# Optimization experiments

Measured on AMD Instinct MI355X. Metric: run time of the kernel, lower is better.

The kernel has to match this reference:

```python
import jax, jax.numpy as jnp
import numpy as np

N = 1024            # number of proposals (128 proposals x 8 images)
D_APP = 2048        # appearance feature dim
D_K = 128           # key/query/value dim
D_G = 128           # geometric embedding dim


def setup_inputs() -> dict:
    key = jax.random.key(0)
    ks = jax.random.split(key, 10)
    s_app = 1.0 / np.sqrt(D_APP)
    s_geo = 1.0 / np.sqrt(D_G)
    return {
        "app_feature": jax.random.normal(ks[0], (N, D_APP), jnp.float32),
        "position_embedding": jax.random.normal(ks[1], (N, N, D_G), jnp.float32),
        "WQ_w": jax.random.normal(ks[2], (D_K, D_APP), jnp.float32) * s_app,
        "WQ_b": jax.random.normal(ks[3], (D_K,), jnp.float32) * 0.01,
        "WK_w": jax.random.normal(ks[4], (D_K, D_APP), jnp.float32) * s_app,
        "WK_b": jax.random.normal(ks[5], (D_K,), jnp.float32) * 0.01,
        "WV_w": jax.random.normal(ks[6], (D_K, D_APP), jnp.float32) * s_app,
        "WV_b": jax.random.normal(ks[7], (D_K,), jnp.float32) * 0.01,
        "WG_w": jax.random.normal(ks[8], (1, D_G), jnp.float32) * s_geo,
        "WG_b": jax.random.normal(ks[9], (1,), jnp.float32) * 0.01,
    }


def reference(app_feature, position_embedding,
              WQ_w, WQ_b, WK_w, WK_b, WV_w, WV_b, WG_w, WG_b):
    n = app_feature.shape[0]
    dim_k = WQ_w.shape[0]
    # projections: (N, D_K)
    w_q = app_feature @ WQ_w.T + WQ_b
    w_k = app_feature @ WK_w.T + WK_b
    w_v = app_feature @ WV_w.T + WV_b
    # appearance scores: (N, N)
    scaled_dot = (w_q @ w_k.T) / jnp.sqrt(jnp.asarray(dim_k, app_feature.dtype))
    # geometric bias: Linear(D_G -> 1) + ReLU, reshaped to (N, N)
    w_g = jax.nn.relu(jnp.einsum('mng,g->mn', position_embedding, WG_w[0]) + WG_b[0])
    # additive bias then row-softmax
    w_mn = jax.nn.softmax(scaled_dot + w_g, axis=1)
    return w_mn @ w_v  # (N, D_K)
```

## Files before the change

kernel.cpp:

```cpp
#include <hip/hip_runtime.h>
#include <math.h>

#define N_PROP 1024
#define DAPP   2048
#define DK     128

__global__ __launch_bounds__(256) void init_bias_kernel(
    const float* __restrict__ bQ, const float* __restrict__ bK,
    const float* __restrict__ bV,
    float* __restrict__ Q, float* __restrict__ K, float* __restrict__ V) {
  int i = blockIdx.x * 256 + threadIdx.x;
  if (i < N_PROP * DK) {
    int c = i & (DK - 1);
    Q[i] = bQ[c];
    K[i] = bK[c];
    V[i] = bV[c];
  }
}

#define BM 64
#define BN 64
#define KC 32
#define KSPLIT_CHUNK 512

__global__ __launch_bounds__(256) void proj_kernel(
    const float* __restrict__ X,
    const float* __restrict__ WQ, const float* __restrict__ WK,
    const float* __restrict__ WV,
    float* __restrict__ Q, float* __restrict__ K, float* __restrict__ V) {
  __shared__ __attribute__((aligned(16))) float As[KC][BM + 4];
  __shared__ __attribute__((aligned(16))) float Bs[KC][BN + 4];

  const int nt = blockIdx.x;
  const int mt = blockIdx.y;
  const int kz = blockIdx.z;
  const int row0 = mt * BM;
  const int proj = nt >> 1;
  const int col0 = (nt & 1) * 64;

  const float* __restrict__ W = (proj == 0) ? WQ : ((proj == 1) ? WK : WV);
  float* __restrict__ O = (proj == 0) ? Q : ((proj == 1) ? K : V);

  const int t  = threadIdx.x;
  const int tx = t & 15, ty = t >> 4;
  const int kk = t & 31, mm = t >> 5;

  float acc[4][4] = {};

  const int k0base = kz * KSPLIT_CHUNK;
  for (int k0 = k0base; k0 < k0base + KSPLIT_CHUNK; k0 += KC) {
    __syncthreads();
#pragma unroll
    for (int r = 0; r < 8; ++r) {
      As[kk][mm + r * 8] = X[(size_t)(row0 + mm + r * 8) * DAPP + k0 + kk];
      Bs[kk][mm + r * 8] = W[(size_t)(col0 + mm + r * 8) * DAPP + k0 + kk];
    }
    __syncthreads();
#pragma unroll
    for (int k = 0; k < KC; ++k) {
      float4 a = *(const float4*)&As[k][ty * 4];
      float4 b = *(const float4*)&Bs[k][tx * 4];
      acc[0][0] += a.x * b.x; acc[0][1] += a.x * b.y; acc[0][2] += a.x * b.z; acc[0][3] += a.x * b.w;
      acc[1][0] += a.y * b.x; acc[1][1] += a.y * b.y; acc[1][2] += a.y * b.z; acc[1][3] += a.y * b.w;
      acc[2][0] += a.z * b.x; acc[2][1] += a.z * b.y; acc[2][2] += a.z * b.z; acc[2][3] += a.z * b.w;
      acc[3][0] += a.w * b.x; acc[3][1] += a.w * b.y; acc[3][2] += a.w * b.z; acc[3][3] += a.w * b.w;
    }
  }

#pragma unroll
  for (int i = 0; i < 4; ++i)
#pragma unroll
    for (int j = 0; j < 4; ++j)
      atomicAdd(&O[(size_t)(row0 + ty * 4 + i) * DK + col0 + tx * 4 + j],
                acc[i][j]);
}

__global__ __launch_bounds__(256) void score_kernel(
    const float* __restrict__ Q, const float* __restrict__ Kmat,
    float* __restrict__ S) {
  __shared__ __attribute__((aligned(16))) float As[KC][BM + 4];
  __shared__ __attribute__((aligned(16))) float Bs[KC][BN + 4];

  const int col0 = blockIdx.x * BN;
  const int row0 = blockIdx.y * BM;
  const int t  = threadIdx.x;
  const int tx = t & 15, ty = t >> 4;
  const int kk = t & 31, mm = t >> 5;

  float acc[4][4] = {};

  for (int k0 = 0; k0 < DK; k0 += KC) {
    __syncthreads();
#pragma unroll
    for (int r = 0; r < 8; ++r) {
      As[kk][mm + r * 8] = Q[(size_t)(row0 + mm + r * 8) * DK + k0 + kk];
      Bs[kk][mm + r * 8] = Kmat[(size_t)(col0 + mm + r * 8) * DK + k0 + kk];
    }
    __syncthreads();
#pragma unroll
    for (int k = 0; k < KC; ++k) {
      float4 a = *(const float4*)&As[k][ty * 4];
      float4 b = *(const float4*)&Bs[k][tx * 4];
      acc[0][0] += a.x * b.x; acc[0][1] += a.x * b.y; acc[0][2] += a.x * b.z; acc[0][3] += a.x * b.w;
      acc[1][0] += a.y * b.x; acc[1][1] += a.y * b.y; acc[1][2] += a.y * b.z; acc[1][3] += a.y * b.w;
      acc[2][0] += a.z * b.x; acc[2][1] += a.z * b.y; acc[2][2] += a.z * b.z; acc[2][3] += a.z * b.w;
      acc[3][0] += a.w * b.x; acc[3][1] += a.w * b.y; acc[3][2] += a.w * b.z; acc[3][3] += a.w * b.w;
    }
  }

  const float scale = 0.08838834764831845f;
#pragma unroll
  for (int i = 0; i < 4; ++i)
#pragma unroll
    for (int j = 0; j < 4; ++j)
      S[(size_t)(row0 + ty * 4 + i) * N_PROP + col0 + tx * 4 + j] =
          acc[i][j] * scale;
}

__global__ __launch_bounds__(256) void fused_gsm_pv_kernel(
    const float* __restrict__ pos, const float* __restrict__ S,
    const float* __restrict__ V, const float* __restrict__ wg,
    const float* __restrict__ bg, float* __restrict__ out) {
  __shared__ __attribute__((aligned(16))) float p[N_PROP];
  __shared__ __attribute__((aligned(16))) float4 accs[256];
  __shared__ float wred[4];

  const int m = blockIdx.x;
  const int t = threadIdx.x;
  const int l  = t & 31;
  const int hw = t >> 5;

  const float4 w4 = *(const float4*)&wg[l * 4];
  const float bG = bg[0];

  {
    const float* __restrict__ pr =
        pos + (size_t)m * N_PROP * DK + (size_t)(hw * 4) * DK + (l << 2);
#pragma unroll 4
    for (int it = 0; it < 32; ++it, pr += 32 * DK) {
      const float4 p0 = *(const float4*)(pr);
      const float4 p1 = *(const float4*)(pr + DK);
      const float4 p2 = *(const float4*)(pr + 2 * DK);
      const float4 p3 = *(const float4*)(pr + 3 * DK);

      float d0 = fmaf(p0.x, w4.x, fmaf(p0.y, w4.y, fmaf(p0.z, w4.z, p0.w * w4.w)));
      float d1 = fmaf(p1.x, w4.x, fmaf(p1.y, w4.y, fmaf(p1.z, w4.z, p1.w * w4.w)));
      float d2 = fmaf(p2.x, w4.x, fmaf(p2.y, w4.y, fmaf(p2.z, w4.z, p2.w * w4.w)));
      float d3 = fmaf(p3.x, w4.x, fmaf(p3.y, w4.y, fmaf(p3.z, w4.z, p3.w * w4.w)));

#pragma unroll
      for (int off = 16; off; off >>= 1) {
        d0 += __shfl_xor(d0, off, 64);
        d1 += __shfl_xor(d1, off, 64);
        d2 += __shfl_xor(d2, off, 64);
        d3 += __shfl_xor(d3, off, 64);
      }
      if (l == 0) {
        float4 g;
        g.x = fmaxf(d0 + bG, 0.0f);
        g.y = fmaxf(d1 + bG, 0.0f);
        g.z = fmaxf(d2 + bG, 0.0f);
        g.w = fmaxf(d3 + bG, 0.0f);
        *(float4*)&p[hw * 4 + it * 32] = g;
      }
    }
  }
  __syncthreads();

  const float4 sr = ((const float4*)(S + (size_t)m * N_PROP))[t];
  const float4 gr = ((const float4*)p)[t];
  const float4 s4 = make_float4(sr.x + gr.x, sr.y + gr.y, sr.z + gr.z, sr.w + gr.w);

  float mx = fmaxf(fmaxf(s4.x, s4.y), fmaxf(s4.z, s4.w));
#pragma unroll
  for (int off = 32; off; off >>= 1) mx = fmaxf(mx, __shfl_xor(mx, off, 64));
  if ((t & 63) == 0) wred[t >> 6] = mx;
  __syncthreads();
  mx = fmaxf(fmaxf(wred[0], wred[1]), fmaxf(wred[2], wred[3]));

  const float e0 = __expf(s4.x - mx), e1 = __expf(s4.y - mx);
  const float e2 = __expf(s4.z - mx), e3 = __expf(s4.w - mx);
  float sum = e0 + e1 + e2 + e3;
#pragma unroll
  for (int off = 32; off; off >>= 1) sum += __shfl_xor(sum, off, 64);
  __syncthreads();
  ((float4*)p)[t] = make_float4(e0, e1, e2, e3);
  if ((t & 63) == 0) wred[t >> 6] = sum;
  __syncthreads();
  sum = wred[0] + wred[1] + wred[2] + wred[3];
  const float inv = 1.0f / sum;

  const int dq = (t & 31) << 2;
  const int ng = t >> 5;
  float4 acc = make_float4(0.f, 0.f, 0.f, 0.f);
  for (int n = ng; n < N_PROP; n += 32) {
    const float pw0 = p[n];
    const float pw1 = p[n + 8];
    const float pw2 = p[n + 16];
    const float pw3 = p[n + 24];
    const float4 v0 = *(const float4*)&V[(size_t)n * DK + dq];
    const float4 v1 = *(const float4*)&V[(size_t)(n + 8) * DK + dq];
    const float4 v2 = *(const float4*)&V[(size_t)(n + 16) * DK + dq];
    const float4 v3 = *(const float4*)&V[(size_t)(n + 24) * DK + dq];
    acc.x += pw0 * v0.x + pw1 * v1.x + pw2 * v2.x + pw3 * v3.x;
    acc.y += pw0 * v0.y + pw1 * v1.y + pw2 * v2.y + pw3 * v3.y;
    acc.z += pw0 * v0.z + pw1 * v1.z + pw2 * v2.z + pw3 * v3.z;
    acc.w += pw0 * v0.w + pw1 * v1.w + pw2 * v2.w + pw3 * v3.w;
  }
  accs[t] = acc;
  __syncthreads();
  if (t < 32) {
    float4 r = accs[t];
#pragma unroll
    for (int g = 1; g < 8; ++g) {
      const float4 o = accs[t + g * 32];
      r.x += o.x; r.y += o.y; r.z += o.z; r.w += o.w;
    }
    r.x *= inv; r.y *= inv; r.z *= inv; r.w *= inv;
    *(float4*)&out[(size_t)m * DK + (t << 2)] = r;
  }
}

extern "C" void kernel_launch(void* const* d_in, const int* in_sizes, int n_in,
                              void* d_out, int out_size, void* d_ws,
                              size_t ws_size, hipStream_t stream) {
  const float* app = (const float*)d_in[0];
  const float* pos = (const float*)d_in[1];
  const float* WQw = (const float*)d_in[2];
  const float* WQb = (const float*)d_in[3];
  const float* WKw = (const float*)d_in[4];
  const float* WKb = (const float*)d_in[5];
  const float* WVw = (const float*)d_in[6];
  const float* WVb = (const float*)d_in[7];
  const float* WGw = (const float*)d_in[8];
  const float* WGb = (const float*)d_in[9];
  float* out = (float*)d_out;

  float* ws = (float*)d_ws;
  float* Q = ws;
  float* K = ws + 131072;
  float* V = ws + 262144;
  float* S = ws + 393216;

  init_bias_kernel<<<dim3(512), dim3(256), 0, stream>>>(WQb, WKb, WVb, Q, K, V);

  proj_kernel<<<dim3(6, 16, 4), dim3(256), 0, stream>>>(app, WQw, WKw, WVw,
                                                        Q, K, V);

  score_kernel<<<dim3(16, 16), dim3(256), 0, stream>>>(Q, K, S);

  fused_gsm_pv_kernel<<<dim3(1024), dim3(256), 0, stream>>>(pos, S, V,
                                                            WGw, WGb, out);
}
```

Baseline: 768.6 us.

## Fuse QK^T score computation into the per-row geometric softmax kernel

Drops the separate tiled score GEMM and the S buffer. Each row block now computes its q·k dot products inline, reusing the same shuffle-reduction pattern as the geometric bias, so the S write/read and one kernel launch go away. The catch is that every row block rereads the full K matrix (512KB, likely L2 resident) and does extra shuffles alongside the position-embedding stream, which is the main memory-bound cost.

```diff
diff --git a/kernel.cpp b/kernel.cpp
--- a/kernel.cpp
+++ b/kernel.cpp
@@ -75,52 +75,11 @@
                 acc[i][j]);
 }
 
-__global__ __launch_bounds__(256) void score_kernel(
-    const float* __restrict__ Q, const float* __restrict__ Kmat,
-    float* __restrict__ S) {
-  __shared__ __attribute__((aligned(16))) float As[KC][BM + 4];
-  __shared__ __attribute__((aligned(16))) float Bs[KC][BN + 4];
-
-  const int col0 = blockIdx.x * BN;
-  const int row0 = blockIdx.y * BM;
-  const int t  = threadIdx.x;
-  const int tx = t & 15, ty = t >> 4;
-  const int kk = t & 31, mm = t >> 5;
-
-  float acc[4][4] = {};
-
-  for (int k0 = 0; k0 < DK; k0 += KC) {
-    __syncthreads();
-#pragma unroll
-    for (int r = 0; r < 8; ++r) {
-      As[kk][mm + r * 8] = Q[(size_t)(row0 + mm + r * 8) * DK + k0 + kk];
-      Bs[kk][mm + r * 8] = Kmat[(size_t)(col0 + mm + r * 8) * DK + k0 + kk];
-    }
-    __syncthreads();
-#pragma unroll
-    for (int k = 0; k < KC; ++k) {
-      float4 a = *(const float4*)&As[k][ty * 4];
-      float4 b = *(const float4*)&Bs[k][tx * 4];
-      acc[0][0] += a.x * b.x; acc[0][1] += a.x * b.y; acc[0][2] += a.x * b.z; acc[0][3] += a.x * b.w;
-      acc[1][0] += a.y * b.x; acc[1][1] += a.y * b.y; acc[1][2] += a.y * b.z; acc[1][3] += a.y * b.w;
-      acc[2][0] += a.z * b.x; acc[2][1] += a.z * b.y; acc[2][2] += a.z * b.z; acc[2][3] += a.z * b.w;
-      acc[3][0] += a.w * b.x; acc[3][1] += a.w * b.y; acc[3][2] += a.w * b.z; acc[3][3] += a.w * b.w;
-    }
-  }
-
-  const float scale = 0.08838834764831845f;
-#pragma unroll
-  for (int i = 0; i < 4; ++i)
-#pragma unroll
-    for (int j = 0; j < 4; ++j)
-      S[(size_t)(row0 + ty * 4 + i) * N_PROP + col0 + tx * 4 + j] =
-          acc[i][j] * scale;
-}
-
-__global__ __launch_bounds__(256) void fused_gsm_pv_kernel(
-    const float* __restrict__ pos, const float* __restrict__ S,
-    const float* __restrict__ V, const float* __restrict__ wg,
-    const float* __restrict__ bg, float* __restrict__ out) {
+__global__ __launch_bounds__(256) void mega_row_kernel(
+    const float* __restrict__ pos, const float* __restrict__ Q,
+    const float* __restrict__ Kmat, const float* __restrict__ V,
+    const float* __restrict__ wg, const float* __restrict__ bg,
+    float* __restrict__ out) {
   __shared__ __attribute__((aligned(16))) float p[N_PROP];
   __shared__ __attribute__((aligned(16))) float4 accs[256];
   __shared__ float wred[4];
@@ -131,45 +90,58 @@
   const int hw = t >> 5;
 
   const float4 w4 = *(const float4*)&wg[l * 4];
+  const float4 q4 = *(const float4*)&Q[(size_t)m * DK + l * 4];
   const float bG = bg[0];
+  const float scale = 0.08838834764831845f;
 
   {
     const float* __restrict__ pr =
         pos + (size_t)m * N_PROP * DK + (size_t)(hw * 4) * DK + (l << 2);
-#pragma unroll 4
-    for (int it = 0; it < 32; ++it, pr += 32 * DK) {
+    const float* __restrict__ kr = Kmat + (size_t)(hw * 4) * DK + (l << 2);
+#pragma unroll 2
+    for (int it = 0; it < 32; ++it, pr += 32 * DK, kr += 32 * DK) {
       const float4 p0 = *(const float4*)(pr);
       const float4 p1 = *(const float4*)(pr + DK);
       const float4 p2 = *(const float4*)(pr + 2 * DK);
       const float4 p3 = *(const float4*)(pr + 3 * DK);
-
-      float d0 = fmaf(p0.x, w4.x, fmaf(p0.y, w4.y, fmaf(p0.z, w4.z, p0.w * w4.w)));
-      float d1 = fmaf(p1.x, w4.x, fmaf(p1.y, w4.y, fmaf(p1.z, w4.z, p1.w * w4.w)));
-      float d2 = fmaf(p2.x, w4.x, fmaf(p2.y, w4.y, fmaf(p2.z, w4.z, p2.w * w4.w)));
-      float d3 = fmaf(p3.x, w4.x, fmaf(p3.y, w4.y, fmaf(p3.z, w4.z, p3.w * w4.w)));
+      const float4 k0 = *(const float4*)(kr);
+      const float4 k1 = *(const float4*)(kr + DK);
+      const float4 k2 = *(const float4*)(kr + 2 * DK);
+      const float4 k3 = *(const float4*)(kr + 3 * DK);
+
+      float g0 = fmaf(p0.x, w4.x, fmaf(p0.y, w4.y, fmaf(p0.z, w4.z, p0.w * w4.w)));
+      float g1 = fmaf(p1.x, w4.x, fmaf(p1.y, w4.y, fmaf(p1.z, w4.z, p1.w * w4.w)));
+      float g2 = fmaf(p2.x, w4.x, fmaf(p2.y, w4.y, fmaf(p2.z, w4.z, p2.w * w4.w)));
+      float g3 = fmaf(p3.x, w4.x, fmaf(p3.y, w4.y, fmaf(p3.z, w4.z, p3.w * w4.w)));
+      float s0 = fmaf(k0.x, q4.x, fmaf(k0.y, q4.y, fmaf(k0.z, q4.z, k0.w * q4.w)));
+      float s1 = fmaf(k1.x, q4.x, fmaf(k1.y, q4.y, fmaf(k1.z, q4.z, k1.w * q4.w)));
+      float s2 = fmaf(k2.x, q4.x, fmaf(k2.y, q4.y, fmaf(k2.z, q4.z, k2.w * q4.w)));
+      float s3 = fmaf(k3.x, q4.x, fmaf(k3.y, q4.y, fmaf(k3.z, q4.z, k3.w * q4.w)));
 
 #pragma unroll
       for (int off = 16; off; off >>= 1) {
-        d0 += __shfl_xor(d0, off, 64);
-        d1 += __shfl_xor(d1, off, 64);
-        d2 += __shfl_xor(d2, off, 64);
-        d3 += __shfl_xor(d3, off, 64);
+        g0 += __shfl_xor(g0, off, 64);
+        g1 += __shfl_xor(g1, off, 64);
+        g2 += __shfl_xor(g2, off, 64);
+        g3 += __shfl_xor(g3, off, 64);
+        s0 += __shfl_xor(s0, off, 64);
+        s1 += __shfl_xor(s1, off, 64);
+        s2 += __shfl_xor(s2, off, 64);
+        s3 += __shfl_xor(s3, off, 64);
       }
       if (l == 0) {
-        float4 g;
-        g.x = fmaxf(d0 + bG, 0.0f);
-        g.y = fmaxf(d1 + bG, 0.0f);
-        g.z = fmaxf(d2 + bG, 0.0f);
-        g.w = fmaxf(d3 + bG, 0.0f);
-        *(float4*)&p[hw * 4 + it * 32] = g;
+        float4 lg;
+        lg.x = fmaf(s0, scale, fmaxf(g0 + bG, 0.0f));
+        lg.y = fmaf(s1, scale, fmaxf(g1 + bG, 0.0f));
+        lg.z = fmaf(s2, scale, fmaxf(g2 + bG, 0.0f));
+        lg.w = fmaf(s3, scale, fmaxf(g3 + bG, 0.0f));
+        *(float4*)&p[hw * 4 + it * 32] = lg;
       }
     }
   }
   __syncthreads();
 
-  const float4 sr = ((const float4*)(S + (size_t)m * N_PROP))[t];
-  const float4 gr = ((const float4*)p)[t];
-  const float4 s4 = make_float4(sr.x + gr.x, sr.y + gr.y, sr.z + gr.z, sr.w + gr.w);
+  const float4 s4 = ((const float4*)p)[t];
 
   float mx = fmaxf(fmaxf(s4.x, s4.y), fmaxf(s4.z, s4.w));
 #pragma unroll
@@ -240,15 +212,12 @@
   float* Q = ws;
   float* K = ws + 131072;
   float* V = ws + 262144;
-  float* S = ws + 393216;
 
   init_bias_kernel<<<dim3(512), dim3(256), 0, stream>>>(WQb, WKb, WVb, Q, K, V);
 
   proj_kernel<<<dim3(6, 16, 4), dim3(256), 0, stream>>>(app, WQw, WKw, WVw,
                                                         Q, K, V);
 
-  score_kernel<<<dim3(16, 16), dim3(256), 0, stream>>>(Q, K, S);
-
-  fused_gsm_pv_kernel<<<dim3(1024), dim3(256), 0, stream>>>(pos, S, V,
-                                                            WGw, WGb, out);
-}
+  mega_row_kernel<<<dim3(1024), dim3(256), 0, stream>>>(pos, Q, K, V,
+                                                        WGw, WGb, out);
+}
```

Result: no change. 764.9 us (-0.5%).
